# Kernel tuning notes

Hardware: AMD Instinct MI355X
Metric: run time of the kernel (lower is better)

## Reference

```python
import jax, jax.numpy as jnp
import numpy as np
from jax import lax

NUM_HEADS = 4
EPS = 1e-12  # torch F.normalize eps


def _dwconv3(x, w):
    # depthwise 3x3 conv, padding 1; w: (C,1,3,3)
    return lax.conv_general_dilated(
        x, w, window_strides=(1, 1), padding=((1, 1), (1, 1)),
        dimension_numbers=('NCHW', 'OIHW', 'NCHW'),
        feature_group_count=w.shape[0])


def _make_qkv(x, w_qkv, w_dw):
    # 1x1 conv (GEMM over channels) then depthwise 3x3
    y = jnp.einsum('bchw,oc->bohw', x, w_qkv)
    y = _dwconv3(y, w_dw)
    b, c3, h, w = y.shape
    c = c3 // 3
    q, k, v = jnp.split(y, 3, axis=1)
    rs = lambda t: t.reshape(b, NUM_HEADS, c // NUM_HEADS, h * w)
    return rs(q), rs(k), rs(v)


def _l2norm(t):
    # F.normalize(t, dim=-1): t / max(||t||_2, eps)
    n = jnp.sqrt(jnp.sum(t * t, axis=-1, keepdims=True))
    return t / jnp.maximum(n, EPS)


def _attend(q, k, v, temperature):
    # channel-wise attention: scores are (b, h, d, d)
    scores = jnp.einsum('bhdn,bhen->bhde', q, k) * temperature
    attn = jax.nn.softmax(scores, axis=-1)
    return jnp.einsum('bhde,bhen->bhdn', attn, v), attn


def setup_inputs() -> dict:
    key = jax.random.key(0)
    ks = jax.random.split(key, 8)
    B, C, H, W = 4, 192, 128, 128
    C3 = 3 * C
    return {
        'e': jax.random.normal(ks[0], (B, C, H, W), jnp.float32),
        'd': jax.random.normal(ks[1], (B, C, H, W), jnp.float32),
        'temperature': jnp.ones((1, NUM_HEADS, 1, 1), jnp.float32),
        'w_qkv': jax.random.normal(ks[2], (C3, C), jnp.float32) * 0.05,
        'w_dw': jax.random.normal(ks[3], (C3, 1, 3, 3), jnp.float32) * 0.1,
        'w_p1': jax.random.normal(ks[4], (C, C), jnp.float32) * 0.05,
        'w_p2': jax.random.normal(ks[5], (C, C), jnp.float32) * 0.05,
        'w_p3': jax.random.normal(ks[6], (C, C), jnp.float32) * 0.05,
        'w_p4': jax.random.normal(ks[7], (C, C), jnp.float32) * 0.05,
    }


def reference(e, d, temperature, w_qkv, w_dw, w_p1, w_p2, w_p3, w_p4):
    b, c, h, w = e.shape
    q_e, k_e, v_e = _make_qkv(e, w_qkv, w_dw)
    q_d, k_d, v_d = _make_qkv(d, w_qkv, w_dw)
    q_e, k_e = _l2norm(q_e), _l2norm(k_e)
    q_d, k_d = _l2norm(q_d), _l2norm(k_d)

    proj = lambda o, wp: jnp.einsum('bchw,oc->bohw', o.reshape(b, c, h, w), wp)

    out_ee, _ = _attend(q_e, k_e, v_e, temperature)
    out_dd, _ = _attend(q_d, k_d, v_d, temperature)
    intra_e = proj(out_ee, w_p1)
    intra_d = proj(out_dd, w_p2)

    out_ed, _ = _attend(q_e, k_d, v_d, temperature)
    # cross d->e: replicate torch's squeeze(0) (no-op unless b==1)
    scores_de = jnp.einsum('bhdn,bhen->bhde', q_d, k_e) * temperature
    attn_de = jax.nn.softmax(scores_de, axis=-1)
    if attn_de.shape[0] == 1:
        attn_de = attn_de[0]
    out_de = jnp.einsum('...de,bhen->bhdn', attn_de, v_e)
    inter_ed = proj(out_ed, w_p3)
    inter_de = proj(out_de, w_p4)
    return (intra_e, intra_d, inter_ed, inter_de)
```

## Files before the change

kernel.cpp:

```cpp
#include <hip/hip_runtime.h>

#define N_PIX 16384
#define CC 192
#define C3 576
#define KTOT 192
#define NCH 32
#define CHUNK 512

typedef __bf16 bf16_t;
typedef bf16_t bf16x4 __attribute__((ext_vector_type(4)));
typedef bf16_t bf16x8 __attribute__((ext_vector_type(8)));
typedef float f32x4 __attribute__((ext_vector_type(4)));

struct WPtrs { const float* p[4]; };
struct GArgs { const float* W[16]; long xoff[16]; int sel[16]; };

template <typename XT, typename YT>
__global__ __launch_bounds__(256) void gemm_k192(GArgs ga,
    const XT* __restrict__ X0, const XT* __restrict__ X1,
    YT* __restrict__ Y, long sY)
{
    __shared__ __align__(16) bf16_t Wl[64][200];
    __shared__ __align__(16) bf16_t Xl[128][36];
    const int bt = blockIdx.z;
    const float* __restrict__ W = ga.W[bt];
    const XT* __restrict__ Xb = (ga.sel[bt] ? X1 : X0) + ga.xoff[bt];
    YT* __restrict__ Yb = Y + (long)bt * sY;
    const int m0 = blockIdx.y * 64, n0 = blockIdx.x * 128;
    const int tid = threadIdx.x;
    const int w = tid >> 6;
    const int gi = (tid >> 4) & 3;
    const int li = tid & 15;
    const int kb4 = tid >> 5;
    const int nb4 = tid & 31;

    f32x4 xf[4];
    bf16x4 xh[4];

    auto loadX = [&](int t) {
        const XT* p = Xb + (long)(32 * t + 4 * kb4) * N_PIX + n0 + 4 * nb4;
        #pragma unroll
        for (int j = 0; j < 4; ++j) {
            if constexpr (sizeof(XT) == 4)
                xf[j] = *(const f32x4*)(p + (long)j * N_PIX);
            else
                xh[j] = *(const bf16x4*)(p + (long)j * N_PIX);
        }
    };
    auto writeX = [&]() {
        #pragma unroll
        for (int i = 0; i < 4; ++i) {
            bf16x4 v;
            if constexpr (sizeof(XT) == 4)
                v = bf16x4{ (bf16_t)xf[0][i], (bf16_t)xf[1][i],
                            (bf16_t)xf[2][i], (bf16_t)xf[3][i] };
            else
                v = bf16x4{ xh[0][i], xh[1][i], xh[2][i], xh[3][i] };
            *(bf16x4*)&Xl[4 * nb4 + i][4 * kb4] = v;
        }
    };

    loadX(0);
    {
        const int wr = tid >> 2, wkb = (tid & 3) * 48;
        #pragma unroll
        for (int j = 0; j < 6; ++j) {
            const float* wp0 = W + (long)(m0 + wr) * KTOT + wkb + 8 * j;
            float4 a = *(const float4*)(wp0);
            float4 b = *(const float4*)(wp0 + 4);
            bf16x8 v = { (bf16_t)a.x, (bf16_t)a.y, (bf16_t)a.z, (bf16_t)a.w,
                         (bf16_t)b.x, (bf16_t)b.y, (bf16_t)b.z, (bf16_t)b.w };
            *(bf16x8*)&Wl[wr][wkb + 8 * j] = v;
        }
    }

    f32x4 acc[4][2];
    #pragma unroll
    for (int i = 0; i < 4; ++i)
        #pragma unroll
        for (int j = 0; j < 2; ++j) acc[i][j] = 0.f;

    for (int t = 0; t < 6; ++t) {
        const int kb = 32 * t;
        writeX();
        if (t < 5) loadX(t + 1);
        __syncthreads();
        bf16x8 af[4], bfr[2];
        #pragma unroll
        for (int mi = 0; mi < 4; ++mi) {
            bf16x4 lo = *(const bf16x4*)&Wl[16 * mi + li][kb + 4 * gi];
            bf16x4 hi = *(const bf16x4*)&Wl[16 * mi + li][kb + 16 + 4 * gi];
            af[mi] = __builtin_shufflevector(lo, hi, 0, 1, 2, 3, 4, 5, 6, 7);
        }
        #pragma unroll
        for (int ni = 0; ni < 2; ++ni) {
            const int n = 32 * w + 16 * ni + li;
            bf16x4 lo = *(const bf16x4*)&Xl[n][4 * gi];
            bf16x4 hi = *(const bf16x4*)&Xl[n][16 + 4 * gi];
            bfr[ni] = __builtin_shufflevector(lo, hi, 0, 1, 2, 3, 4, 5, 6, 7);
        }
        #pragma unroll
        for (int mi = 0; mi < 4; ++mi)
            #pragma unroll
            for (int ni = 0; ni < 2; ++ni)
                acc[mi][ni] = __builtin_amdgcn_mfma_f32_16x16x32_bf16(
                    af[mi], bfr[ni], acc[mi][ni], 0, 0, 0);
        __syncthreads();
    }
    #pragma unroll
    for (int mi = 0; mi < 4; ++mi)
        #pragma unroll
        for (int ni = 0; ni < 2; ++ni) {
            const int n = n0 + 32 * w + 16 * ni + li;
            #pragma unroll
            for (int r = 0; r < 4; ++r) {
                const int m = m0 + 16 * mi + 4 * gi + r;
                Yb[(long)m * N_PIX + n] = (YT)acc[mi][ni][r];
            }
        }
}

__global__ __launch_bounds__(256) void dwconv3b(const bf16_t* __restrict__ Yin,
    const float* __restrict__ wdw, bf16_t* __restrict__ Z,
    float* __restrict__ invn)
{
    const int ch = blockIdx.x, sb = blockIdx.y;
    const int tid = threadIdx.x;
    const int x0 = (tid & 15) << 3;
    const int y0 = (tid >> 4) << 3;
    const bf16_t* __restrict__ inp = Yin + (long)(sb * C3 + ch) * N_PIX;
    bf16_t* __restrict__ outp = Z + (long)(sb * C3 + ch) * N_PIX;
    const float* wch = wdw + ch * 9;
    const float w00 = wch[0], w01 = wch[1], w02 = wch[2];
    const float w10 = wch[3], w11 = wch[4], w12 = wch[5];
    const float w20 = wch[6], w21 = wch[7], w22 = wch[8];
    const bool hasL = (x0 > 0), hasR = (x0 < 120);
    float A[10], B[10], Cr[10];
    auto loadrow = [&](int yy, float* r) {
        if (yy < 0 || yy > 127) {
            #pragma unroll
            for (int i = 0; i < 10; ++i) r[i] = 0.f;
            return;
        }
        const bf16_t* p = inp + (yy << 7);
        bf16x8 v = *(const bf16x8*)(p + x0);
        #pragma unroll
        for (int j = 0; j < 8; ++j) r[1 + j] = (float)v[j];
        r[0] = hasL ? (float)p[x0 - 1] : 0.f;
        r[9] = hasR ? (float)p[x0 + 8] : 0.f;
    };
    loadrow(y0 - 1, A);
    loadrow(y0,     B);
    float ss = 0.f;
    #pragma unroll
    for (int r = 0; r < 8; ++r) {
        loadrow(y0 + r + 1, Cr);
        bf16x8 ov;
        #pragma unroll
        for (int i = 0; i < 8; ++i) {
            float s;
            s = fmaf(w00, A[i],  fmaf(w01, A[i + 1],  w02 * A[i + 2]));
            s = fmaf(w10, B[i],  fmaf(w11, B[i + 1],  fmaf(w12, B[i + 2], s)));
            s = fmaf(w20, Cr[i], fmaf(w21, Cr[i + 1], fmaf(w22, Cr[i + 2], s)));
            ov[i] = (bf16_t)s;
            const float vb = (float)ov[i];
            ss = fmaf(vb, vb, ss);
        }
        *(bf16x8*)(outp + ((y0 + r) << 7) + x0) = ov;
        #pragma unroll
        for (int i = 0; i < 10; ++i) { A[i] = B[i]; B[i] = Cr[i]; }
    }
    if (ch < 384) {
        #pragma unroll
        for (int off = 32; off > 0; off >>= 1) ss += __shfl_down(ss, off);
        __shared__ float red[4];
        if ((tid & 63) == 0) red[tid >> 6] = ss;
        __syncthreads();
        if (tid == 0) {
            const float t = red[0] + red[1] + red[2] + red[3];
            const int row = (sb >> 2) * 1536 + (sb & 3) * 384 + ch;
            invn[row] = 1.f / fmaxf(sqrtf(t), 1e-12f);
        }
    }
}

__global__ __launch_bounds__(256) void scores_mfma(const bf16_t* __restrict__ Z,
                                                   float* __restrict__ part)
{
    const int c = blockIdx.x;
    const int bh = blockIdx.y;
    const int b = bh >> 2, h = bh & 3;
    __shared__ __align__(16) bf16_t T[4][48][72];
    const int tid = threadIdx.x;
    const int m = tid >> 6;
    const int gi = (tid >> 4) & 3, li = tid & 15;
    const int qs = (m == 1 || m == 3) ? 1 : 0;
    const int ks = (m == 1 || m == 2) ? 1 : 0;
    f32x4 acc[3][3];
    #pragma unroll
    for (int i = 0; i < 3; ++i)
        #pragma unroll
        for (int j = 0; j < 3; ++j) acc[i][j] = 0.f;

    const int nbase = c * CHUNK;
    for (int k0 = 0; k0 < CHUNK; k0 += 64) {
        __syncthreads();
        for (int l = tid; l < 1536; l += 256) {
            const int t = l / 384;
            const int rem = l - t * 384;
            const int r = rem >> 3, s = rem & 7;
            const int sidx = (t < 2) ? t : (t - 2);
            const int qk = (t < 2) ? 0 : 1;
            const bf16_t* gp = Z + ((long)((sidx * 4 + b) * C3 + qk * 192 + h * 48 + r)) * N_PIX
                                 + nbase + k0 + s * 8;
            *(bf16x8*)&T[t][r][s * 8] = *(const bf16x8*)gp;
        }
        __syncthreads();
        #pragma unroll
        for (int k2 = 0; k2 < 64; k2 += 32) {
            bf16x8 af[3], bfr[3];
            #pragma unroll
            for (int i = 0; i < 3; ++i) {
                bf16x4 lo = *(const bf16x4*)&T[qs][16 * i + li][k2 + 4 * gi];
                bf16x4 hi = *(const bf16x4*)&T[qs][16 * i + li][k2 + 16 + 4 * gi];
                af[i] = __builtin_shufflevector(lo, hi, 0, 1, 2, 3, 4, 5, 6, 7);
            }
            #pragma unroll
            for (int j = 0; j < 3; ++j) {
                bf16x4 lo = *(const bf16x4*)&T[2 + ks][16 * j + li][k2 + 4 * gi];
                bf16x4 hi = *(const bf16x4*)&T[2 + ks][16 * j + li][k2 + 16 + 4 * gi];
                bfr[j] = __builtin_shufflevector(lo, hi, 0, 1, 2, 3, 4, 5, 6, 7);
            }
            #pragma unroll
            for (int i = 0; i < 3; ++i)
                #pragma unroll
                for (int j = 0; j < 3; ++j)
                    acc[i][j] = __builtin_amdgcn_mfma_f32_16x16x32_bf16(
                        af[i], bfr[j], acc[i][j], 0, 0, 0);
        }
    }
    const long base = ((long)(m * 16 + bh) * NCH + c) * 2304;
    #pragma unroll
    for (int i = 0; i < 3; ++i)
        #pragma unroll
        for (int j = 0; j < 3; ++j) {
            const int e = 16 * j + li;
            #pragma unroll
            for (int r = 0; r < 4; ++r) {
                const int d = 16 * i + 4 * gi + r;
                part[base + d * 48 + e] = acc[i][j][r];
            }
        }
}

__global__ __launch_bounds__(256) void reduce_softmax(const float* __restrict__ part,
    const float* __restrict__ invn, const float* __restrict__ temp,
    float* __restrict__ attn)
{
    const int mbh = blockIdx.x;
    const int m = mbh >> 4, b = (mbh >> 2) & 3, h = mbh & 3;
    const int qs = (m == 1 || m == 3) ? 1 : 0;
    const int ks = (m == 1 || m == 2) ? 1 : 0;
    __shared__ float sm[48][48];
    const int tid = threadIdx.x;
    const long pbase = (long)mbh * NCH * 2304;
    const float T = temp[h];
    for (int idx = tid; idx < 2304; idx += 256) {
        float v = 0.f;
        #pragma unroll 8
        for (int c = 0; c < NCH; ++c) v += part[pbase + c * 2304 + idx];
        const int d = idx / 48, e = idx % 48;
        const float iq = invn[(qs * 4 + b) * 384 + h * 48 + d];
        const float ik = invn[(ks * 4 + b) * 384 + 192 + h * 48 + e];
        sm[d][e] = v * iq * ik * T;
    }
    __syncthreads();
    if (tid < 48) {
        float mx = -1e30f;
        #pragma unroll
        for (int e = 0; e < 48; ++e) mx = fmaxf(mx, sm[tid][e]);
        float sum = 0.f;
        #pragma unroll
        for (int e = 0; e < 48; ++e) {
            const float v = __expf(sm[tid][e] - mx);
            sm[tid][e] = v;
            sum += v;
        }
        const float inv = 1.f / sum;
        const long abase = (long)mbh * 2304 + (long)tid * 48;
        #pragma unroll
        for (int e = 0; e < 48; ++e) attn[abase + e] = sm[tid][e] * inv;
    }
}

__global__ __launch_bounds__(256) void make_M(const float* __restrict__ attn,
                                              WPtrs wp, float* __restrict__ M)
{
    const int h = blockIdx.x & 3;
    const int b = (blockIdx.x >> 2) & 3;
    const int m = blockIdx.x >> 4;
    __shared__ float A[48][48];
    const int tid = threadIdx.x;
    if (m == 3) {
        for (int l = tid; l < 2304; l += 256) {
            float s = 0.f;
            #pragma unroll
            for (int bb = 0; bb < 16; ++bb)
                s += attn[(long)(48 + bb) * 2304 + l];
            A[l / 48][l % 48] = s;
        }
    } else {
        const long ab = (long)(m * 16 + b * 4 + h) * 2304;
        for (int l = tid; l < 2304; l += 256)
            A[l / 48][l % 48] = attn[ab + l];
    }
    __syncthreads();
    const float* W = wp.p[m];
    float* Mo = M + (long)(m * 4 + b) * 192 * 192;
    for (int o = tid >> 4; o < 192; o += 16) {
        const float* wrow = W + (long)o * 192 + h * 48;
        for (int e2 = tid & 15; e2 < 48; e2 += 16) {
            float s = 0.f;
            #pragma unroll
            for (int d = 0; d < 48; ++d) s = fmaf(wrow[d], A[d][e2], s);
            Mo[(long)o * 192 + h * 48 + e2] = s;
        }
    }
}

extern "C" void kernel_launch(void* const* d_in, const int* in_sizes, int n_in,
                              void* d_out, int out_size, void* d_ws, size_t ws_size,
                              hipStream_t stream)
{
    const float* e     = (const float*)d_in[0];
    const float* d     = (const float*)d_in[1];
    const float* temp  = (const float*)d_in[2];
    const float* w_qkv = (const float*)d_in[3];
    const float* w_dw  = (const float*)d_in[4];
    const float* w_p1  = (const float*)d_in[5];
    const float* w_p2  = (const float*)d_in[6];
    const float* w_p3  = (const float*)d_in[7];
    const float* w_p4  = (const float*)d_in[8];
    float* out = (float*)d_out;
    float* ws  = (float*)d_ws;

    bf16_t* zraw = (bf16_t*)ws;
    bf16_t* zb   = (bf16_t*)(ws + 37748736L);
    float* attn  = ws + 75497472L;
    float* invn  = ws + 75644928L;
    float* part  = ws;
    float* Mmat  = ws + 8388608L;

    const long sXin = (long)CC * N_PIX;
    const long sQKV = (long)C3 * N_PIX;

    GArgs gq{};
    for (int bt = 0; bt < 8; ++bt) {
        gq.W[bt] = w_qkv;
        gq.xoff[bt] = (long)(bt & 3) * sXin;
        gq.sel[bt] = bt >> 2;
    }
    gemm_k192<float, bf16_t><<<dim3(128, 9, 8), 256, 0, stream>>>(gq, e, d, zraw, sQKV);
    dwconv3b<<<dim3(C3, 8), 256, 0, stream>>>(zraw, w_dw, zb, invn);
    scores_mfma<<<dim3(NCH, 16), 256, 0, stream>>>(zb, part);
    reduce_softmax<<<dim3(64), 256, 0, stream>>>(part, invn, temp, attn);
    WPtrs wpj; wpj.p[0] = w_p1; wpj.p[1] = w_p2; wpj.p[2] = w_p3; wpj.p[3] = w_p4;
    make_M<<<dim3(64), 256, 0, stream>>>(attn, wpj, Mmat);
    GArgs gm{};
    for (int bt = 0; bt < 16; ++bt) {
        const int m = bt >> 2, b = bt & 3;
        const int ks = (m == 1 || m == 2) ? 1 : 0;
        gm.W[bt] = Mmat + (long)bt * 192 * 192;
        gm.xoff[bt] = ((long)((ks * 4 + b) * C3 + 384)) * N_PIX;
        gm.sel[bt] = 0;
    }
    gemm_k192<bf16_t, float><<<dim3(128, 3, 16), 256, 0, stream>>>(gm, zb, zb, out, sXin);
}
```

Before: 368.4 us.

## Double-buffer X tiles with swizzled LDS layout and reorder projection GEMM batches

```diff
diff --git a/kernel.cpp b/kernel.cpp
--- a/kernel.cpp
+++ b/kernel.cpp
@@ -13,19 +13,19 @@
 typedef float f32x4 __attribute__((ext_vector_type(4)));
 
 struct WPtrs { const float* p[4]; };
-struct GArgs { const float* W[16]; long xoff[16]; int sel[16]; };
+struct GArgs { const float* W[16]; long xoff[16]; long yoff[16]; int sel[16]; };
 
 template <typename XT, typename YT>
 __global__ __launch_bounds__(256) void gemm_k192(GArgs ga,
     const XT* __restrict__ X0, const XT* __restrict__ X1,
-    YT* __restrict__ Y, long sY)
+    YT* __restrict__ Y, long )
 {
     __shared__ __align__(16) bf16_t Wl[64][200];
-    __shared__ __align__(16) bf16_t Xl[128][36];
+    __shared__ __align__(16) bf16_t Xl[2][128][36];
     const int bt = blockIdx.z;
     const float* __restrict__ W = ga.W[bt];
     const XT* __restrict__ Xb = (ga.sel[bt] ? X1 : X0) + ga.xoff[bt];
-    YT* __restrict__ Yb = Y + (long)bt * sY;
+    YT* __restrict__ Yb = Y + ga.yoff[bt];
     const int m0 = blockIdx.y * 64, n0 = blockIdx.x * 128;
     const int tid = threadIdx.x;
     const int w = tid >> 6;
@@ -33,6 +33,7 @@
     const int li = tid & 15;
     const int kb4 = tid >> 5;
     const int nb4 = tid & 31;
+    const int wcol = 4 * (kb4 ^ (nb4 & 7));
 
     f32x4 xf[4];
     bf16x4 xh[4];
@@ -47,7 +48,7 @@
                 xh[j] = *(const bf16x4*)(p + (long)j * N_PIX);
         }
     };
-    auto writeX = [&]() {
+    auto writeX = [&](int buf) {
         #pragma unroll
         for (int i = 0; i < 4; ++i) {
             bf16x4 v;
@@ -56,7 +57,7 @@
                             (bf16_t)xf[2][i], (bf16_t)xf[3][i] };
             else
                 v = bf16x4{ xh[0][i], xh[1][i], xh[2][i], xh[3][i] };
-            *(bf16x4*)&Xl[4 * nb4 + i][4 * kb4] = v;
+            *(bf16x4*)&Xl[buf][4 * nb4 + i][wcol] = v;
         }
     };
 
@@ -73,6 +74,8 @@
             *(bf16x8*)&Wl[wr][wkb + 8 * j] = v;
         }
     }
+    writeX(0);
+    __syncthreads();
 
     f32x4 acc[4][2];
     #pragma unroll
@@ -80,11 +83,11 @@
         #pragma unroll
         for (int j = 0; j < 2; ++j) acc[i][j] = 0.f;
 
+    #pragma unroll
     for (int t = 0; t < 6; ++t) {
+        const int cur = t & 1;
+        if (t < 5) loadX(t + 1);
         const int kb = 32 * t;
-        writeX();
-        if (t < 5) loadX(t + 1);
-        __syncthreads();
         bf16x8 af[4], bfr[2];
         #pragma unroll
         for (int mi = 0; mi < 4; ++mi) {
@@ -95,8 +98,9 @@
         #pragma unroll
         for (int ni = 0; ni < 2; ++ni) {
             const int n = 32 * w + 16 * ni + li;
-            bf16x4 lo = *(const bf16x4*)&Xl[n][4 * gi];
-            bf16x4 hi = *(const bf16x4*)&Xl[n][16 + 4 * gi];
+            const int swz = (n >> 2) & 7;
+            bf16x4 lo = *(const bf16x4*)&Xl[cur][n][4 * (gi ^ swz)];
+            bf16x4 hi = *(const bf16x4*)&Xl[cur][n][4 * ((gi + 4) ^ swz)];
             bfr[ni] = __builtin_shufflevector(lo, hi, 0, 1, 2, 3, 4, 5, 6, 7);
         }
         #pragma unroll
@@ -105,6 +109,7 @@
             for (int ni = 0; ni < 2; ++ni)
                 acc[mi][ni] = __builtin_amdgcn_mfma_f32_16x16x32_bf16(
                     af[mi], bfr[ni], acc[mi][ni], 0, 0, 0);
+        if (t < 5) writeX(cur ^ 1);
         __syncthreads();
     }
     #pragma unroll
@@ -358,21 +363,25 @@
     for (int bt = 0; bt < 8; ++bt) {
         gq.W[bt] = w_qkv;
         gq.xoff[bt] = (long)(bt & 3) * sXin;
+        gq.yoff[bt] = (long)bt * sQKV;
         gq.sel[bt] = bt >> 2;
     }
-    gemm_k192<float, bf16_t><<<dim3(128, 9, 8), 256, 0, stream>>>(gq, e, d, zraw, sQKV);
+    gemm_k192<float, bf16_t><<<dim3(128, 9, 8), 256, 0, stream>>>(gq, e, d, zraw, 0);
     dwconv3b<<<dim3(C3, 8), 256, 0, stream>>>(zraw, w_dw, zb, invn);
     scores_mfma<<<dim3(NCH, 16), 256, 0, stream>>>(zb, part);
     reduce_softmax<<<dim3(64), 256, 0, stream>>>(part, invn, temp, attn);
     WPtrs wpj; wpj.p[0] = w_p1; wpj.p[1] = w_p2; wpj.p[2] = w_p3; wpj.p[3] = w_p4;
     make_M<<<dim3(64), 256, 0, stream>>>(attn, wpj, Mmat);
     GArgs gm{};
-    for (int bt = 0; bt < 16; ++bt) {
-        const int m = bt >> 2, b = bt & 3;
+    const int morder[16] = {0,3,0,3,0,3,0,3, 1,2,1,2,1,2,1,2};
+    const int border[16] = {0,0,1,1,2,2,3,3, 0,0,1,1,2,2,3,3};
+    for (int z = 0; z < 16; ++z) {
+        const int m = morder[z], b = border[z];
         const int ks = (m == 1 || m == 2) ? 1 : 0;
-        gm.W[bt] = Mmat + (long)bt * 192 * 192;
-        gm.xoff[bt] = ((long)((ks * 4 + b) * C3 + 384)) * N_PIX;
-        gm.sel[bt] = 0;
-    }
-    gemm_k192<bf16_t, float><<<dim3(128, 3, 16), 256, 0, stream>>>(gm, zb, zb, out, sXin);
-}
+        gm.W[z] = Mmat + (long)(m * 4 + b) * 192 * 192;
+        gm.xoff[z] = ((long)((ks * 4 + b) * C3 + 384)) * N_PIX;
+        gm.yoff[z] = (long)(m * 4 + b) * sXin;
+        gm.sel[z] = 0;
+    }
+    gemm_k192<bf16_t, float><<<dim3(128, 3, 16), 256, 0, stream>>>(gm, zb, zb, out, 0);
+}
```

Result: slower. 377.1 us (+2.4%).
